# Performance work log

Measured on AMD Instinct MI355X. Metric: run time of the kernel, lower is better.

## Reference

```python
import jax, jax.numpy as jnp
import numpy as np

CONV_NUM = 8
CONV_SIZE = 96
HIDDEN = 768  # = CONV_NUM * CONV_SIZE
MAX_LEN = 128


def get_entity(x, s, e):
    # x: [B, L, H]; mean of x[i, s[i]:max(e[i], s[i]+1)] per sample (ragged gather+mean)
    e = jnp.maximum(e, s + 1)
    pos = jnp.arange(x.shape[1])  # [L]
    mask = (pos[None, :] >= s[:, None]) & (pos[None, :] < e[:, None])  # [B, L]
    m = mask.astype(x.dtype)
    return jnp.einsum('blh,bl->bh', x, m) / jnp.sum(m, axis=1, keepdims=True)


def feature_abstract(head_ent, tail_ent, x, fc_W, fc_b):
    # head_ent/tail_ent: [B, HIDDEN] -> per-sample conv filters; x: [B, HIDDEN]
    B = x.shape[0]
    wh = head_ent.reshape(B * CONV_NUM, 1, 1, CONV_SIZE)
    wt = tail_ent.reshape(B * CONV_NUM, 1, 1, CONV_SIZE)
    lhs = x.reshape(1, B, 1, HIDDEN)  # NCHW, groups=B -> per-sample correlation
    h = jax.nn.relu(jax.lax.conv_general_dilated(lhs, wh, (1, 1), 'VALID', feature_group_count=B))
    t = jax.nn.relu(jax.lax.conv_general_dilated(lhs, wt, (1, 1), 'VALID', feature_group_count=B))
    # h,t: [1, B*CONV_NUM, 1, T] with T = HIDDEN - CONV_SIZE + 1
    ht = jnp.concatenate([h, t], axis=3).reshape(B * CONV_NUM, -1)  # [B*cn, 2T]
    ht = ht.reshape(B * CONV_NUM, -1, 2).mean(axis=-1)  # AvgPool1d(k=2, s=2) -> [B*cn, T]
    flat = ht.reshape(B, -1)  # [B, cn*T] (dropout is identity in eval)
    return flat @ fc_W.T + fc_b  # [B, HIDDEN]


def setup_inputs() -> dict:
    key = jax.random.key(0)
    ks = jax.random.split(key, 16)
    Bs, Bq, L, H = 400, 1200, MAX_LEN, HIDDEN

    def spans(k1, k2, B):
        s = jax.random.randint(k1, (B,), 0, 100)
        e = jnp.minimum(s + jax.random.randint(k2, (B,), 1, 20), L)
        return s.astype(jnp.int64), e.astype(jnp.int64)

    s_eh, s_eh_end = spans(ks[0], ks[1], Bs)
    s_et, s_et_end = spans(ks[2], ks[3], Bs)
    q_eh, q_eh_end = spans(ks[4], ks[5], Bq)
    q_et, q_et_end = spans(ks[6], ks[7], Bq)
    fc_in = (H - CONV_SIZE + 1) * CONV_NUM  # 5384
    return {
        'all_support': jax.random.normal(ks[8], (Bs, L, H), jnp.float32),
        'support_emb': jax.random.normal(ks[9], (Bs, H), jnp.float32),
        'all_query': jax.random.normal(ks[10], (Bq, L, H), jnp.float32),
        'query_emb': jax.random.normal(ks[11], (Bq, H), jnp.float32),
        'fc_W': jax.random.normal(ks[12], (H, fc_in), jnp.float32) / np.sqrt(fc_in),
        'fc_b': jnp.zeros((H,), jnp.float32),
        's_eh': s_eh, 's_eh_end': s_eh_end, 's_et': s_et, 's_et_end': s_et_end,
        'q_eh': q_eh, 'q_eh_end': q_eh_end, 'q_et': q_et, 'q_et_end': q_et_end,
        'N': 10, 'K': 5, 'total_Q': 150,
    }


def reference(all_support, support_emb, all_query, query_emb, fc_W, fc_b,
              s_eh, s_eh_end, s_et, s_et_end, q_eh, q_eh_end, q_et, q_et_end,
              N, K, total_Q):
    sh = get_entity(all_support, s_eh, s_eh_end)
    st = get_entity(all_support, s_et, s_et_end)
    qh = get_entity(all_query, q_eh, q_eh_end)
    qt = get_entity(all_query, q_et, q_et_end)

    sup = feature_abstract(sh, st, support_emb, fc_W, fc_b).reshape(-1, N, K, HIDDEN)
    qry = feature_abstract(qh, qt, query_emb, fc_W, fc_b).reshape(-1, total_Q, HIDDEN)

    proto = sup.mean(axis=2)  # [Be, N, H]
    # -||proto - query||^2 over feature dim -> [Be, total_Q, N]
    diff = proto[:, None, :, :] - qry[:, :, None, :]
    logits = -jnp.sum(diff * diff, axis=-1)
    minn = logits.min(axis=-1)
    logits = jnp.concatenate([logits, minn[..., None] - 1.0], axis=2)  # [Be, total_Q, N+1]
    pred = jnp.argmax(logits.reshape(-1, N + 1), axis=1)
    return logits, pred
```

## Files before the change

### kernel.cpp

```cpp
#include <hip/hip_runtime.h>

#define H        768
#define LMAX     128
#define CONV_NUM 8
#define CONV_SIZE 96
#define T_CONV   673
#define FC_IN    5384
#define KP       5408
#define KSTEPS   (KP / 32)
#define N_WAY    10
#define K_SHOT   5
#define TOTAL_Q  150
#define SPLITK   8
#define BS       400
#define BQ       1200
#define MTOT     1600
#define NPROTO   80
#define MA       1280

using s16x8 = __attribute__((ext_vector_type(8))) short;
using f32x4 = __attribute__((ext_vector_type(4))) float;
typedef unsigned short u16;

__device__ __forceinline__ u16 f2bf(float x) {
    unsigned u = __float_as_uint(x);
    u += 0x7FFFu + ((u >> 16) & 1u);
    return (u16)(u >> 16);
}
__device__ __forceinline__ float bf2f(u16 b) { return __uint_as_float(((unsigned)b) << 16); }

__device__ __forceinline__ void gl16(const u16* g, u16* l) {
    __builtin_amdgcn_global_load_lds(
        (const __attribute__((address_space(1))) unsigned int*)g,
        (__attribute__((address_space(3))) unsigned int*)l, 16, 0, 0);
}

#define HTS 678
#define XCS 784
__global__ __launch_bounds__(256, 4) void pre_kernel(
    const float* __restrict__ all_support, const float* __restrict__ all_query,
    const float* __restrict__ support_emb, const float* __restrict__ query_emb,
    const float* __restrict__ fc_W,
    const int* __restrict__ s_eh, const int* __restrict__ s_eh_end,
    const int* __restrict__ s_et, const int* __restrict__ s_et_end,
    const int* __restrict__ q_eh, const int* __restrict__ q_eh_end,
    const int* __restrict__ q_et, const int* __restrict__ q_et_end,
    u16* __restrict__ flatS, u16* __restrict__ A_bf,
    u16* __restrict__ Wh)
{
    int bid = blockIdx.x;
    int tid = threadIdx.x;

    if (bid >= MTOT) {
        int r = bid - MTOT;
        for (int j = tid; j < KP; j += 256) {
            float v = (j < FC_IN) ? fc_W[(size_t)r * FC_IN + j] : 0.f;
            Wh[(size_t)r * KP + j] = f2bf(v);
        }
        return;
    }

    __shared__ u16 htb[16 * HTS];
    __shared__ u16 filt_h[16 * 96];
    __shared__ u16 filt_l[16 * 96];
    __shared__ u16 xcs[8][XCS];
    float* xs = (float*)htb;

    int b = bid;
    const float* src;
    int sh, eh, st, et;
    if (b < BS) {
        src = all_support + (size_t)b * LMAX * H;
        sh = s_eh[b]; eh = s_eh_end[b]; st = s_et[b]; et = s_et_end[b];
    } else {
        int m = b - BS;
        src = all_query + (size_t)m * LMAX * H;
        sh = q_eh[m]; eh = q_eh_end[m]; st = q_et[m]; et = q_et_end[m];
    }
    if (eh < sh + 1) eh = sh + 1;
    if (et < st + 1) et = st + 1;

    {
        float a0 = 0.f, a1 = 0.f, a2 = 0.f;
        for (int r = sh; r < eh; ++r) {
            const float* row = src + (size_t)r * H;
            a0 += row[tid]; a1 += row[tid + 256]; a2 += row[tid + 512];
        }
        float rc = 1.0f / (float)(eh - sh);
        float m0 = a0 * rc, m1 = a1 * rc, m2 = a2 * rc;
        u16 h0 = f2bf(m0), h1 = f2bf(m1), h2 = f2bf(m2);
        filt_h[tid] = h0;       filt_l[tid] = f2bf(m0 - bf2f(h0));
        filt_h[tid + 256] = h1; filt_l[tid + 256] = f2bf(m1 - bf2f(h1));
        filt_h[tid + 512] = h2; filt_l[tid + 512] = f2bf(m2 - bf2f(h2));
        a0 = a1 = a2 = 0.f;
        for (int r = st; r < et; ++r) {
            const float* row = src + (size_t)r * H;
            a0 += row[tid]; a1 += row[tid + 256]; a2 += row[tid + 512];
        }
        rc = 1.0f / (float)(et - st);
        m0 = a0 * rc; m1 = a1 * rc; m2 = a2 * rc;
        h0 = f2bf(m0); h1 = f2bf(m1); h2 = f2bf(m2);
        filt_h[tid + 768] = h0;  filt_l[tid + 768] = f2bf(m0 - bf2f(h0));
        filt_h[tid + 1024] = h1; filt_l[tid + 1024] = f2bf(m1 - bf2f(h1));
        filt_h[tid + 1280] = h2; filt_l[tid + 1280] = f2bf(m2 - bf2f(h2));
    }
    const float* xsrc = (b < BS) ? (support_emb + (size_t)b * H)
                                 : (query_emb + (size_t)(b - BS) * H);
    if (tid < 192)
        *(float4*)&xs[tid * 4] = *(const float4*)&xsrc[tid * 4];
    if (tid >= 192 && tid < 200) {
        int o = 768 + (tid - 192) * 4;
        xs[o] = 0.f; xs[o + 1] = 0.f; xs[o + 2] = 0.f; xs[o + 3] = 0.f;
    }
    __syncthreads();

    #pragma unroll 1
    for (int c = 0; c < 8; ++c)
        for (int i = tid; i < XCS; i += 256)
            xcs[c][i] = f2bf(xs[i + c]);
    __syncthreads();

    {
        int lane = tid & 63, wv = tid >> 6;
        int n = lane & 15, g = lane >> 4;
        int afo = n * 96 + g * 8;
        s16x8 fh0 = *(const s16x8*)&filt_h[afo];
        s16x8 fh1 = *(const s16x8*)&filt_h[afo + 32];
        s16x8 fh2 = *(const s16x8*)&filt_h[afo + 64];
        s16x8 fl0 = *(const s16x8*)&filt_l[afo];
        s16x8 fl1 = *(const s16x8*)&filt_l[afo + 32];
        s16x8 fl2 = *(const s16x8*)&filt_l[afo + 64];
        const u16* xrow = &xcs[n & 7][g * 8 + (n & 8)];
        #pragma unroll 1
        for (int nt = wv; nt < 43; nt += 4) {
            const u16* xp = xrow + nt * 16;
            s16x8 x0 = *(const s16x8*)(xp);
            s16x8 x1 = *(const s16x8*)(xp + 32);
            s16x8 x2 = *(const s16x8*)(xp + 64);
            f32x4 a = (f32x4){0.f, 0.f, 0.f, 0.f};
            a = __builtin_amdgcn_mfma_f32_16x16x32_bf16(fh0, x0, a, 0, 0, 0);
            a = __builtin_amdgcn_mfma_f32_16x16x32_bf16(fl0, x0, a, 0, 0, 0);
            a = __builtin_amdgcn_mfma_f32_16x16x32_bf16(fh1, x1, a, 0, 0, 0);
            a = __builtin_amdgcn_mfma_f32_16x16x32_bf16(fl1, x1, a, 0, 0, 0);
            a = __builtin_amdgcn_mfma_f32_16x16x32_bf16(fh2, x2, a, 0, 0, 0);
            a = __builtin_amdgcn_mfma_f32_16x16x32_bf16(fl2, x2, a, 0, 0, 0);
            int pcol = nt * 16 + n;
            if (pcol < T_CONV) {
                #pragma unroll
                for (int r = 0; r < 4; ++r)
                    htb[(g * 4 + r) * HTS + pcol] = f2bf(fmaxf(a[r], 0.f));
            }
        }
    }
    __syncthreads();

    u16* oh = (b < BS) ? (flatS + (size_t)b * KP)
                       : (A_bf + (size_t)(NPROTO + b - BS) * KP);
    for (int f = 0; f < CONV_NUM; ++f) {
        for (int j = tid; j < T_CONV; j += 256) {
            int i0 = 2 * j, i1 = 2 * j + 1;
            float v0 = bf2f((i0 < T_CONV) ? htb[f * HTS + i0]
                                          : htb[(8 + f) * HTS + (i0 - T_CONV)]);
            float v1 = bf2f((i1 < T_CONV) ? htb[f * HTS + i1]
                                          : htb[(8 + f) * HTS + (i1 - T_CONV)]);
            oh[f * T_CONV + j] = f2bf(0.5f * (v0 + v1));
        }
    }
    for (int j = FC_IN + tid; j < KP; j += 256) oh[j] = 0;
}

__global__ __launch_bounds__(256) void avg_kernel(
    const u16* __restrict__ flatS, u16* __restrict__ A_bf)
{
    int i = blockIdx.x;
    size_t base = (size_t)i * K_SHOT * KP;
    for (int t = threadIdx.x; t < KP / 8; t += 256) {
        int j = t * 8;
        float s[8] = {0.f, 0.f, 0.f, 0.f, 0.f, 0.f, 0.f, 0.f};
        #pragma unroll
        for (int k = 0; k < K_SHOT; ++k) {
            s16x8 vh = *(const s16x8*)(flatS + base + (size_t)k * KP + j);
            #pragma unroll
            for (int u = 0; u < 8; ++u)
                s[u] += bf2f((u16)vh[u]);
        }
        s16x8 oh;
        #pragma unroll
        for (int u = 0; u < 8; ++u)
            oh[u] = (short)f2bf(s[u] * (1.0f / K_SHOT));
        *(s16x8*)(A_bf + (size_t)i * KP + j) = oh;
    }
}

#define ASEG 8192
#define BSEG 4096
#define BUFU (ASEG + BSEG)

#define STAGE(ks, buf) do {                                     \
    int kb_ = (ks) * 32;                                        \
    u16* L_ = &lds[buf][0];                                     \
    gl16(Ah_g + aoff0 + kb_, L_ + cA0 * 8);                     \
    gl16(Ah_g + aoff1 + kb_, L_ + cA1 * 8);                     \
    gl16(Bh_g + boff  + kb_, L_ + ASEG + cB * 8);               \
} while (0)

__global__ __launch_bounds__(512, 2) void gemm_mfma(
    const u16* __restrict__ Ah_g, const u16* __restrict__ Bh_g,
    float* __restrict__ parts)
{
    __shared__ u16 lds[2][BUFU];

    int tid = threadIdx.x;
    int wg = (blockIdx.x & 7) * 30 + (blockIdx.x >> 3);
    int sk = wg / 30;
    int rem = wg % 30;
    int n0 = (rem / 5) * 128;
    int m0 = (rem % 5) * 256;

    int ks0 = (KSTEPS * sk) / SPLITK;
    int nk = (KSTEPS * (sk + 1)) / SPLITK - ks0;

    int cA0 = tid, cA1 = tid + 512;
    int cB = tid;
    size_t aoff0 = (size_t)(m0 + (cA0 >> 6) * 16 + (cA0 & 15)) * KP + ((cA0 >> 4) & 3) * 8;
    size_t aoff1 = (size_t)(m0 + (cA1 >> 6) * 16 + (cA1 & 15)) * KP + ((cA1 >> 4) & 3) * 8;
    size_t boff  = (size_t)(n0 + (cB >> 6) * 16 + (cB & 15)) * KP + ((cB >> 4) & 3) * 8;

    int w = tid >> 6, lane = tid & 63;
    int wm = w >> 1, wn = w & 1;
    int lfr = ((lane >> 4) * 16 + (lane & 15)) * 8;

    f32x4 acc[4][4];
    #pragma unroll
    for (int i = 0; i < 4; ++i)
        #pragma unroll
        for (int j = 0; j < 4; ++j) acc[i][j] = (f32x4){0.f, 0.f, 0.f, 0.f};

    STAGE(ks0, 0);
    STAGE(ks0 + 1, 1);

    int cur = 0;
    for (int k = 0; k < nk; ++k) {
        if (k + 1 < nk) asm volatile("s_waitcnt vmcnt(3)" ::: "memory");
        else            asm volatile("s_waitcnt vmcnt(0)" ::: "memory");
        __builtin_amdgcn_s_barrier();

        const u16* L = &lds[cur][0];
        s16x8 ah[4], bh[4];
        #pragma unroll
        for (int f = 0; f < 4; ++f) {
            ah[f] = *(const s16x8*)(L + (wm * 4 + f) * 512 + lfr);
            bh[f] = *(const s16x8*)(L + ASEG + (wn * 4 + f) * 512 + lfr);
        }
        asm volatile("s_waitcnt lgkmcnt(0)" ::: "memory");
        __builtin_amdgcn_s_barrier();

        if (k + 2 < nk) STAGE(ks0 + k + 2, cur);

        #pragma unroll
        for (int i = 0; i < 4; ++i)
            #pragma unroll
            for (int j = 0; j < 4; ++j)
                acc[i][j] = __builtin_amdgcn_mfma_f32_16x16x32_bf16(ah[i], bh[j], acc[i][j], 0, 0, 0);
        cur ^= 1;
    }

    int rbase = m0 + wm * 64 + (lane >> 4) * 4;
    int cbase = n0 + wn * 64 + (lane & 15);
    #pragma unroll
    for (int i = 0; i < 4; ++i) {
        int row0 = rbase + i * 16;
        #pragma unroll
        for (int j = 0; j < 4; ++j) {
            int col = cbase + j * 16;
            float* dst = parts + ((size_t)sk * MA + row0) * H + col;
            #pragma unroll
            for (int r = 0; r < 4; ++r)
                dst[(size_t)r * H] = acc[i][j][r];
        }
    }
}

__global__ __launch_bounds__(256) void protofin_kernel(
    const float* __restrict__ parts, const float* __restrict__ bias,
    float* __restrict__ proto)
{
    int i = blockIdx.x;
    int tid = threadIdx.x;
    #pragma unroll
    for (int q = 0; q < 3; ++q) {
        int d = tid + q * 256;
        float s = bias[d];
        #pragma unroll
        for (int sp = 0; sp < SPLITK; ++sp)
            s += parts[((size_t)sp * MA + i) * H + d];
        proto[(size_t)i * H + d] = s;
    }
}

__global__ __launch_bounds__(256) void dist_kernel(
    const float* __restrict__ parts, const float* __restrict__ bias,
    const float* __restrict__ proto, float* __restrict__ outp)
{
    int bid = blockIdx.x;
    int e = bid / TOTAL_Q;
    int tid = threadIdx.x;
    int m = NPROTO + bid;

    float qv[3];
    #pragma unroll
    for (int q = 0; q < 3; ++q) {
        int d = tid + q * 256;
        float s = bias[d];
        #pragma unroll
        for (int sp = 0; sp < SPLITK; ++sp)
            s += parts[((size_t)sp * MA + m) * H + d];
        qv[q] = s;
    }

    __shared__ float red[N_WAY][4];
    __shared__ float lvals[N_WAY];
    int wave = tid >> 6, lane = tid & 63;
    for (int n = 0; n < N_WAY; ++n) {
        const float* pr = proto + (size_t)(e * N_WAY + n) * H;
        float p = 0.f;
        #pragma unroll
        for (int q = 0; q < 3; ++q) {
            int d = tid + q * 256;
            float df = pr[d] - qv[q];
            p = fmaf(df, df, p);
        }
        #pragma unroll
        for (int off = 32; off > 0; off >>= 1)
            p += __shfl_down(p, off);
        if (lane == 0) red[n][wave] = p;
    }
    __syncthreads();
    if (tid < N_WAY) {
        float v = red[tid][0] + red[tid][1] + red[tid][2] + red[tid][3];
        lvals[tid] = -v;
        outp[(size_t)bid * (N_WAY + 1) + tid] = -v;
    }
    __syncthreads();
    if (tid == 0) {
        float mn = lvals[0];
        #pragma unroll
        for (int n = 1; n < N_WAY; ++n) mn = fminf(mn, lvals[n]);
        float last = mn - 1.0f;
        outp[(size_t)bid * (N_WAY + 1) + N_WAY] = last;
        float best = lvals[0];
        int bi = 0;
        for (int n = 1; n < N_WAY; ++n)
            if (lvals[n] > best) { best = lvals[n]; bi = n; }
        if (last > best) bi = N_WAY;
        outp[(size_t)BQ * (N_WAY + 1) + bid] = (float)bi;
    }
}

extern "C" void kernel_launch(void* const* d_in, const int* in_sizes, int n_in,
                              void* d_out, int out_size, void* d_ws, size_t ws_size,
                              hipStream_t stream)
{
    const float* all_support = (const float*)d_in[0];
    const float* support_emb = (const float*)d_in[1];
    const float* all_query   = (const float*)d_in[2];
    const float* query_emb   = (const float*)d_in[3];
    const float* fc_W        = (const float*)d_in[4];
    const float* fc_b        = (const float*)d_in[5];
    const int* s_eh     = (const int*)d_in[6];
    const int* s_eh_end = (const int*)d_in[7];
    const int* s_et     = (const int*)d_in[8];
    const int* s_et_end = (const int*)d_in[9];
    const int* q_eh     = (const int*)d_in[10];
    const int* q_eh_end = (const int*)d_in[11];
    const int* q_et     = (const int*)d_in[12];
    const int* q_et_end = (const int*)d_in[13];

    float* parts = (float*)d_ws;
    float* proto = parts + (size_t)SPLITK * MA * H;
    u16* Wh      = (u16*)(proto + (size_t)NPROTO * H);
    u16* A_bf    = Wh + (size_t)H * KP;
    u16* flatS   = A_bf + (size_t)MA * KP;

    pre_kernel<<<MTOT + H, 256, 0, stream>>>(
        all_support, all_query, support_emb, query_emb, fc_W,
        s_eh, s_eh_end, s_et, s_et_end, q_eh, q_eh_end, q_et, q_et_end,
        flatS, A_bf, Wh);

    avg_kernel<<<NPROTO, 256, 0, stream>>>(flatS, A_bf);

    gemm_mfma<<<240, 512, 0, stream>>>(A_bf, Wh, parts);

    protofin_kernel<<<NPROTO, 256, 0, stream>>>(parts, fc_b, proto);

    dist_kernel<<<BQ, 256, 0, stream>>>(parts, fc_b, proto, (float*)d_out);
}
```

Baseline: 76.67 us.

## Store split-K partials in bf16, widen per-wave GEMM tile, drop cancelling bias

The GEMM now runs 4 waves per block, each computing a 64x128 output tile with more accumulators, instead of 8 waves at 64x64. Split-K partial sums are written as bf16 rather than fp32, halving the traffic into the prototype and distance kernels. The fc bias is removed because it cancels in the squared distance between prototypes and queries. The exchange is lower precision in the summed features, plus higher register pressure and lower occupancy in the GEMM.

```diff
diff --git a/kernel.cpp b/kernel.cpp
--- a/kernel.cpp
+++ b/kernel.cpp
@@ -201,12 +201,15 @@
     u16* L_ = &lds[buf][0];                                     \
     gl16(Ah_g + aoff0 + kb_, L_ + cA0 * 8);                     \
     gl16(Ah_g + aoff1 + kb_, L_ + cA1 * 8);                     \
-    gl16(Bh_g + boff  + kb_, L_ + ASEG + cB * 8);               \
+    gl16(Ah_g + aoff2 + kb_, L_ + cA2 * 8);                     \
+    gl16(Ah_g + aoff3 + kb_, L_ + cA3 * 8);                     \
+    gl16(Bh_g + boff0 + kb_, L_ + ASEG + cB0 * 8);              \
+    gl16(Bh_g + boff1 + kb_, L_ + ASEG + cB1 * 8);              \
 } while (0)
 
-__global__ __launch_bounds__(512, 2) void gemm_mfma(
+__global__ __launch_bounds__(256, 2) void gemm_mfma(
     const u16* __restrict__ Ah_g, const u16* __restrict__ Bh_g,
-    float* __restrict__ parts)
+    u16* __restrict__ partsB)
 {
     __shared__ u16 lds[2][BUFU];
 
@@ -220,38 +223,41 @@
     int ks0 = (KSTEPS * sk) / SPLITK;
     int nk = (KSTEPS * (sk + 1)) / SPLITK - ks0;
 
-    int cA0 = tid, cA1 = tid + 512;
-    int cB = tid;
+    int cA0 = tid, cA1 = tid + 256, cA2 = tid + 512, cA3 = tid + 768;
+    int cB0 = tid, cB1 = tid + 256;
     size_t aoff0 = (size_t)(m0 + (cA0 >> 6) * 16 + (cA0 & 15)) * KP + ((cA0 >> 4) & 3) * 8;
     size_t aoff1 = (size_t)(m0 + (cA1 >> 6) * 16 + (cA1 & 15)) * KP + ((cA1 >> 4) & 3) * 8;
-    size_t boff  = (size_t)(n0 + (cB >> 6) * 16 + (cB & 15)) * KP + ((cB >> 4) & 3) * 8;
+    size_t aoff2 = (size_t)(m0 + (cA2 >> 6) * 16 + (cA2 & 15)) * KP + ((cA2 >> 4) & 3) * 8;
+    size_t aoff3 = (size_t)(m0 + (cA3 >> 6) * 16 + (cA3 & 15)) * KP + ((cA3 >> 4) & 3) * 8;
+    size_t boff0 = (size_t)(n0 + (cB0 >> 6) * 16 + (cB0 & 15)) * KP + ((cB0 >> 4) & 3) * 8;
+    size_t boff1 = (size_t)(n0 + (cB1 >> 6) * 16 + (cB1 & 15)) * KP + ((cB1 >> 4) & 3) * 8;
 
     int w = tid >> 6, lane = tid & 63;
-    int wm = w >> 1, wn = w & 1;
     int lfr = ((lane >> 4) * 16 + (lane & 15)) * 8;
 
-    f32x4 acc[4][4];
+    f32x4 acc[4][8];
     #pragma unroll
     for (int i = 0; i < 4; ++i)
         #pragma unroll
-        for (int j = 0; j < 4; ++j) acc[i][j] = (f32x4){0.f, 0.f, 0.f, 0.f};
+        for (int j = 0; j < 8; ++j) acc[i][j] = (f32x4){0.f, 0.f, 0.f, 0.f};
 
     STAGE(ks0, 0);
     STAGE(ks0 + 1, 1);
 
     int cur = 0;
     for (int k = 0; k < nk; ++k) {
-        if (k + 1 < nk) asm volatile("s_waitcnt vmcnt(3)" ::: "memory");
+        if (k + 1 < nk) asm volatile("s_waitcnt vmcnt(6)" ::: "memory");
         else            asm volatile("s_waitcnt vmcnt(0)" ::: "memory");
         __builtin_amdgcn_s_barrier();
 
         const u16* L = &lds[cur][0];
-        s16x8 ah[4], bh[4];
-        #pragma unroll
-        for (int f = 0; f < 4; ++f) {
-            ah[f] = *(const s16x8*)(L + (wm * 4 + f) * 512 + lfr);
-            bh[f] = *(const s16x8*)(L + ASEG + (wn * 4 + f) * 512 + lfr);
-        }
+        s16x8 ah[4], bh[8];
+        #pragma unroll
+        for (int f = 0; f < 4; ++f)
+            ah[f] = *(const s16x8*)(L + (w * 4 + f) * 512 + lfr);
+        #pragma unroll
+        for (int j = 0; j < 8; ++j)
+            bh[j] = *(const s16x8*)(L + ASEG + j * 512 + lfr);
         asm volatile("s_waitcnt lgkmcnt(0)" ::: "memory");
         __builtin_amdgcn_s_barrier();
 
@@ -260,47 +266,46 @@
         #pragma unroll
         for (int i = 0; i < 4; ++i)
             #pragma unroll
-            for (int j = 0; j < 4; ++j)
+            for (int j = 0; j < 8; ++j)
                 acc[i][j] = __builtin_amdgcn_mfma_f32_16x16x32_bf16(ah[i], bh[j], acc[i][j], 0, 0, 0);
         cur ^= 1;
     }
 
-    int rbase = m0 + wm * 64 + (lane >> 4) * 4;
-    int cbase = n0 + wn * 64 + (lane & 15);
+    int rbase = m0 + w * 64 + (lane >> 4) * 4;
+    int cbase = n0 + (lane & 15);
     #pragma unroll
     for (int i = 0; i < 4; ++i) {
         int row0 = rbase + i * 16;
         #pragma unroll
-        for (int j = 0; j < 4; ++j) {
+        for (int j = 0; j < 8; ++j) {
             int col = cbase + j * 16;
-            float* dst = parts + ((size_t)sk * MA + row0) * H + col;
+            u16* dst = partsB + ((size_t)sk * MA + row0) * H + col;
             #pragma unroll
             for (int r = 0; r < 4; ++r)
-                dst[(size_t)r * H] = acc[i][j][r];
+                dst[(size_t)r * H] = f2bf(acc[i][j][r]);
         }
     }
 }
 
 __global__ __launch_bounds__(256) void protofin_kernel(
-    const float* __restrict__ parts, const float* __restrict__ bias,
-    float* __restrict__ proto)
+    const u16* __restrict__ partsB, float* __restrict__ proto)
 {
     int i = blockIdx.x;
     int tid = threadIdx.x;
     #pragma unroll
     for (int q = 0; q < 3; ++q) {
         int d = tid + q * 256;
-        float s = bias[d];
+        float s = 0.f;
         #pragma unroll
         for (int sp = 0; sp < SPLITK; ++sp)
-            s += parts[((size_t)sp * MA + i) * H + d];
+            s += bf2f(partsB[((size_t)sp * MA + i) * H + d]);
         proto[(size_t)i * H + d] = s;
     }
 }
 
 __global__ __launch_bounds__(256) void dist_kernel(
-    const float* __restrict__ parts, const float* __restrict__ bias,
-    const float* __restrict__ proto, float* __restrict__ outp)
+    const u16* __restrict__ partsB, const float* __restrict__ proto,
+    float* __restrict__ outp)
 {
     int bid = blockIdx.x;
     int e = bid / TOTAL_Q;
@@ -311,10 +316,10 @@
     #pragma unroll
     for (int q = 0; q < 3; ++q) {
         int d = tid + q * 256;
-        float s = bias[d];
+        float s = 0.f;
         #pragma unroll
         for (int sp = 0; sp < SPLITK; ++sp)
-            s += parts[((size_t)sp * MA + m) * H + d];
+            s += bf2f(partsB[((size_t)sp * MA + m) * H + d]);
         qv[q] = s;
     }
 
@@ -366,7 +371,6 @@
     const float* all_query   = (const float*)d_in[2];
     const float* query_emb   = (const float*)d_in[3];
     const float* fc_W        = (const float*)d_in[4];
-    const float* fc_b        = (const float*)d_in[5];
     const int* s_eh     = (const int*)d_in[6];
     const int* s_eh_end = (const int*)d_in[7];
     const int* s_et     = (const int*)d_in[8];
@@ -376,8 +380,8 @@
     const int* q_et     = (const int*)d_in[12];
     const int* q_et_end = (const int*)d_in[13];
 
-    float* parts = (float*)d_ws;
-    float* proto = parts + (size_t)SPLITK * MA * H;
+    u16* partsB  = (u16*)d_ws;
+    float* proto = (float*)(partsB + (size_t)SPLITK * MA * H);
     u16* Wh      = (u16*)(proto + (size_t)NPROTO * H);
     u16* A_bf    = Wh + (size_t)H * KP;
     u16* flatS   = A_bf + (size_t)MA * KP;
@@ -389,9 +393,9 @@
 
     avg_kernel<<<NPROTO, 256, 0, stream>>>(flatS, A_bf);
 
-    gemm_mfma<<<240, 512, 0, stream>>>(A_bf, Wh, parts);
-
-    protofin_kernel<<<NPROTO, 256, 0, stream>>>(parts, fc_b, proto);
-
-    dist_kernel<<<BQ, 256, 0, stream>>>(parts, fc_b, proto, (float*)d_out);
-}
+    gemm_mfma<<<240, 256, 0, stream>>>(A_bf, Wh, partsB);
+
+    protofin_kernel<<<NPROTO, 256, 0, stream>>>(partsB, proto);
+
+    dist_kernel<<<BQ, 256, 0, stream>>>(partsB, proto, (float*)d_out);
+}
```

After: 74.75 us. 1.03x faster.
